# Kernel optimization log

Measured on AMD Instinct MI355X. Metric: run time of the kernel, lower is better.

## Reference

```python
import jax, jax.numpy as jnp
import numpy as np

B, N, D, K = 32, 4096, 128, 512
NPB = 2048          # unique tail nodes per batch (>= K so topk branch is taken)
M = B * NPB         # total unique tail nodes
E = B * N           # total edges
NUM_ENT = 10000


def setup_inputs() -> dict:
    key = jax.random.key(0)
    ks = jax.random.split(key, 18)
    f = lambda k, s: jax.random.normal(k, s, dtype=jnp.float32)
    inp = {
        "q_head": f(ks[0], (B, D)),
        "q_rel": f(ks[1], (B, D)),
        "q_time": f(ks[2], (B, D)),
        "r_neighbor": f(ks[3], (B, N, D)),
        "t_neighbor": f(ks[4], (B, N, D)),
        "time_neighbor": f(ks[5], (B, N, D)),
        "hidden": f(ks[6], (E, D)),
        "tail_emd": jnp.zeros((M, D), jnp.float32),  # scatter out-buffer
    }
    # tail_index: each edge of batch b scatters into that batch's node slab
    local = jax.random.randint(ks[7], (B, N), 0, NPB)
    inp["tail_index"] = (local + jnp.arange(B)[:, None] * NPB).reshape(E).astype(jnp.int32)
    # tail_nodes: [M,3] = (batch id, tail entity, time)
    batch_col = jnp.repeat(jnp.arange(B), NPB)
    tail_col = jax.random.randint(ks[8], (M,), 0, NUM_ENT)
    time_col = jax.random.randint(ks[9], (M,), 0, 365)
    inp["tail_nodes"] = jnp.stack([batch_col, tail_col, time_col], axis=-1).astype(jnp.int32)
    # linear-layer params (torch nn.Linear-style scaling)
    s3, s1 = 1.0 / np.sqrt(3 * D), 1.0 / np.sqrt(D)
    inp["W_q"] = f(ks[10], (3 * D, D)) * s3
    inp["b_q"] = jnp.zeros((D,), jnp.float32)
    inp["W_a"] = f(ks[11], (3 * D, D)) * s3
    inp["b_a"] = jnp.zeros((D,), jnp.float32)
    inp["W_att"] = f(ks[12], (3 * D, 1)) * s3
    inp["b_att"] = jnp.zeros((1,), jnp.float32)
    inp["W_rule"] = f(ks[13], (D, 1)) * s1
    inp["b_rule"] = jnp.zeros((1,), jnp.float32)
    inp["W_out"] = f(ks[14], (D, D)) * s1
    inp["b_out"] = jnp.zeros((D,), jnp.float32)
    return inp


def reference(q_head, q_rel, q_time, r_neighbor, t_neighbor, time_neighbor,
              hidden, tail_emd, tail_index, tail_nodes,
              W_q, b_q, W_a, b_a, W_att, b_att, W_rule, b_rule, W_out, b_out):
    # act = identity (module default). reduce = 'sum'.
    # raw message per edge: [E, D]
    message = (q_head[:, None, :] + r_neighbor + time_neighbor).reshape(E, D)
    # query / neighbor projections
    query = jnp.concatenate([q_head, q_rel, q_time], axis=-1) @ W_q + b_q      # [B, D]
    neigh = jnp.concatenate([r_neighbor, t_neighbor, time_neighbor], -1) @ W_a + b_a  # [B, N, D]
    q = query[:, None, :]
    qa = jnp.concatenate([q * neigh, q - neigh, q + neigh], axis=-1)           # [B, N, 3D]
    att1 = jax.nn.sigmoid(qa @ W_att + b_att).reshape(E, 1)
    att2 = jax.nn.sigmoid(hidden @ W_rule + b_rule)                            # [E, 1]
    att = (att1 + att2) * 0.5
    msg = att * message
    # scatter-sum aggregation over unique tail nodes
    seg = lambda v: jax.ops.segment_sum(v, tail_index, num_segments=M)
    tail_agg = tail_emd + seg(msg)            # scatter(..., out=tail_emd)
    new_hidden = seg(hidden)                  # [M, D]
    agg_att = seg(att[:, 0])                  # [M]
    # per-batch top-k over aggregated attention (each batch has NPB >= K nodes)
    nodes_batch = tail_nodes[:, 0]
    scores = jnp.where(nodes_batch[None, :] == jnp.arange(B)[:, None],
                       agg_att[None, :], -jnp.inf)                             # [B, M]
    _, idx = jax.lax.top_k(scores, K)                                          # [B, K] global node ids
    new_nodes = jnp.stack([tail_nodes[:, 1][idx], tail_nodes[:, 2][idx]], -1)  # [B, K, 2]
    emd = tail_agg[idx]                                                        # [B, K, D]
    hid = new_hidden[idx]                                                      # [B, K, D]
    out_emd = emd @ W_out + b_out                                              # act=identity
    return new_nodes, out_emd, hid
```

## Files before the change

### kernel.cpp

```cpp
#include <hip/hip_runtime.h>
#include <math.h>

#define B 32
#define N 4096
#define D 128
#define KTOP 512
#define NPB 2048
#define MSEG (B * NPB)
#define E (B * N)
#define MAXL 96

__global__ __launch_bounds__(128) void k0_precompute(
    const float* __restrict__ qh, const float* __restrict__ qr,
    const float* __restrict__ qt, const float* __restrict__ Wq,
    const float* __restrict__ bq, const float* __restrict__ Wa,
    const float* __restrict__ ba, const float* __restrict__ Watt,
    const float* __restrict__ batt, double* __restrict__ vws,
    double* __restrict__ c2ws) {
  int b = blockIdx.x, d = threadIdx.x;
  __shared__ double u[128];
  __shared__ double red[128];
  const float* qhb = qh + b * 128;
  const float* qrb = qr + b * 128;
  const float* qtb = qt + b * 128;
  double acc = (double)bq[d];
  for (int i = 0; i < 128; ++i) acc += (double)qhb[i] * (double)Wq[i * 128 + d];
  for (int i = 0; i < 128; ++i) acc += (double)qrb[i] * (double)Wq[(128 + i) * 128 + d];
  for (int i = 0; i < 128; ++i) acc += (double)qtb[i] * (double)Wq[(256 + i) * 128 + d];
  double w1 = (double)Watt[d], w2 = (double)Watt[128 + d], w3 = (double)Watt[256 + d];
  double ud = acc * w1 - w2 + w3;
  u[d] = ud;
  red[d] = acc * (w2 + w3) + (double)ba[d] * ud;
  __syncthreads();
  for (int s = 64; s > 0; s >>= 1) {
    if (d < s) red[d] += red[d + s];
    __syncthreads();
  }
  if (d == 0) c2ws[b] = red[0] + (double)batt[0];
  for (int i = d; i < 384; i += 128) {
    double vv = 0.0;
    for (int dd = 0; dd < 128; ++dd) vv += (double)Wa[i * 128 + dd] * u[dd];
    vws[b * 384 + i] = vv;
  }
}

__global__ __launch_bounds__(256) void k1_att(
    const float* __restrict__ r, const float* __restrict__ t,
    const float* __restrict__ tm, const float* __restrict__ hidden,
    const float* __restrict__ Wrule, const float* __restrict__ brule,
    const double* __restrict__ vws, const double* __restrict__ c2ws,
    float* __restrict__ attw) {
  int wid = threadIdx.x >> 6;
  int lane = threadIdx.x & 63;
  int e = blockIdx.x * 4 + wid;
  int b = e >> 12;
  size_t eo = (size_t)e * 128;
  const float2* r2 = (const float2*)(r + eo);
  const float2* t2 = (const float2*)(t + eo);
  const float2* m2 = (const float2*)(tm + eo);
  const float2* h2 = (const float2*)(hidden + eo);
  const double2* vb = (const double2*)(vws + b * 384);
  float2 ra = r2[lane], ta = t2[lane], ma = m2[lane], ha = h2[lane];
  double2 v0 = vb[lane], v1 = vb[64 + lane], v2 = vb[128 + lane];
  float2 wr = ((const float2*)Wrule)[lane];
  double p1 = (double)ra.x * v0.x + (double)ra.y * v0.y +
              (double)ta.x * v1.x + (double)ta.y * v1.y +
              (double)ma.x * v2.x + (double)ma.y * v2.y;
  double p2 = (double)ha.x * (double)wr.x + (double)ha.y * (double)wr.y;
  for (int off = 32; off > 0; off >>= 1) {
    p1 += __shfl_xor(p1, off);
    p2 += __shfl_xor(p2, off);
  }
  if (lane == 0) {
    double l1 = p1 + c2ws[b];
    double l2 = p2 + (double)brule[0];
    double a1 = 1.0 / (1.0 + exp(-l1));
    double a2 = 1.0 / (1.0 + exp(-l2));
    attw[e] = (float)(0.5 * (a1 + a2));
  }
}

__global__ __launch_bounds__(256) void k_hist(const int* __restrict__ tidx,
                                              int* __restrict__ counts) {
  int e = blockIdx.x * 256 + threadIdx.x;
  atomicAdd(&counts[tidx[e]], 1);
}

__global__ __launch_bounds__(256) void k_scanA(const int* __restrict__ counts,
                                               int* __restrict__ off,
                                               int* __restrict__ bsum) {
  __shared__ int sd[256];
  int tid = threadIdx.x;
  int g = blockIdx.x * 256 + tid;
  int c = counts[g];
  sd[tid] = c;
  __syncthreads();
  for (int s = 1; s < 256; s <<= 1) {
    int tv = (tid >= s) ? sd[tid - s] : 0;
    __syncthreads();
    sd[tid] += tv;
    __syncthreads();
  }
  off[g] = sd[tid] - c;
  if (tid == 255) bsum[blockIdx.x] = sd[255];
}

__global__ __launch_bounds__(256) void k_scanB(const int* __restrict__ bsum,
                                               int* __restrict__ boff) {
  __shared__ int sd[256];
  int tid = threadIdx.x;
  int c = bsum[tid];
  sd[tid] = c;
  __syncthreads();
  for (int s = 1; s < 256; s <<= 1) {
    int tv = (tid >= s) ? sd[tid - s] : 0;
    __syncthreads();
    sd[tid] += tv;
    __syncthreads();
  }
  boff[tid] = sd[tid] - c;
}

__global__ __launch_bounds__(256) void k_scanC(int* __restrict__ off,
                                               const int* __restrict__ boff,
                                               int* __restrict__ cur) {
  int g = blockIdx.x * 256 + threadIdx.x;
  int o = off[g] + boff[g >> 8];
  off[g] = o;
  cur[g] = o;
}

__global__ __launch_bounds__(256) void k_scatter(const int* __restrict__ tidx,
                                                 int* __restrict__ cur,
                                                 int* __restrict__ lists) {
  int e = blockIdx.x * 256 + threadIdx.x;
  int m = tidx[e];
  int pos = atomicAdd(&cur[m], 1);
  lists[pos] = e;
}

__global__ __launch_bounds__(128) void k5_agg(
    const float* __restrict__ r, const float* __restrict__ tm,
    const float* __restrict__ hidden, const float* __restrict__ qh,
    const float* __restrict__ tail_emd, const float* __restrict__ attw,
    const int* __restrict__ counts, const int* __restrict__ offs,
    const int* __restrict__ lists, float* __restrict__ tail_agg,
    float* __restrict__ new_hidden, float* __restrict__ agg_att) {
  int m = blockIdx.x;
  int d = threadIdx.x;
  int b = m >> 11;
  __shared__ int s_list[MAXL];
  __shared__ float s_att[MAXL];
  int cnt = counts[m];
  if (cnt > MAXL) cnt = MAXL;
  int off = offs[m];
  if (d < cnt) s_list[d] = lists[off + d];
  __syncthreads();
  if (d == 0) {
    for (int i = 1; i < cnt; i++) {
      int key = s_list[i];
      int j = i - 1;
      while (j >= 0 && s_list[j] > key) {
        s_list[j + 1] = s_list[j];
        j--;
      }
      s_list[j + 1] = key;
    }
  }
  __syncthreads();
  if (d < cnt) s_att[d] = attw[s_list[d]];
  __syncthreads();
  if (d == 0) {
    float s = 0.f;
    for (int j = 0; j < cnt; j++) s += s_att[j];
    agg_att[m] = s;
  }
  float qhd = qh[b * 128 + d];
  float accT = tail_emd[(size_t)m * 128 + d];
  float accH = 0.f;
  for (int j = 0; j < cnt; j++) {
    int e = s_list[j];
    float a = s_att[j];
    size_t eo = (size_t)e * 128 + d;
    float message = (qhd + r[eo]) + tm[eo];
    accT += a * message;
    accH += hidden[eo];
  }
  tail_agg[(size_t)m * 128 + d] = accT;
  new_hidden[(size_t)m * 128 + d] = accH;
}

__global__ __launch_bounds__(1024) void k6_topk(
    const float* __restrict__ agg_att, const int* __restrict__ tail_nodes,
    float* __restrict__ out_nodes, int* __restrict__ idxw) {
  __shared__ float v[2048];
  __shared__ int ix[2048];
  int b = blockIdx.x, tid = threadIdx.x;
  for (int s = tid; s < 2048; s += 1024) {
    v[s] = agg_att[b * 2048 + s];
    ix[s] = s;
  }
  __syncthreads();
  for (int k = 2; k <= 2048; k <<= 1) {
    for (int j = k >> 1; j > 0; j >>= 1) {
      for (int t = tid; t < 2048; t += 1024) {
        int p = t ^ j;
        if (p > t) {
          bool asc = ((t & k) == 0);
          float vt = v[t], vp = v[p];
          int it = ix[t], ip = ix[p];
          bool before_p = (vp > vt) || (vp == vt && ip < it);
          if (before_p == asc) {
            v[t] = vp; v[p] = vt;
            ix[t] = ip; ix[p] = it;
          }
        }
      }
      __syncthreads();
    }
  }
  if (tid < KTOP) {
    int s = ix[tid];
    int gm = b * 2048 + s;
    out_nodes[(b * KTOP + tid) * 2 + 0] = (float)tail_nodes[gm * 3 + 1];
    out_nodes[(b * KTOP + tid) * 2 + 1] = (float)tail_nodes[gm * 3 + 2];
    idxw[b * KTOP + tid] = gm;
  }
}

__global__ __launch_bounds__(256) void k7_out(
    const float* __restrict__ tail_agg, const float* __restrict__ new_hidden,
    const float* __restrict__ Wout, const float* __restrict__ bout,
    const int* __restrict__ idxw, float* __restrict__ out_emd,
    float* __restrict__ out_hid) {
  __shared__ float Ws[16384];
  __shared__ float es[256];
  int tid = threadIdx.x;
  int sub = tid >> 7, d = tid & 127;
  for (int i = tid; i < 16384; i += 256) Ws[i] = Wout[i];
  int base = blockIdx.x * 32;
  float bo = bout[d];
  for (int j = 0; j < 32; j += 2) {
    int row = base + j + sub;
    int m = idxw[row];
    __syncthreads();
    es[sub * 128 + d] = tail_agg[(size_t)m * 128 + d];
    __syncthreads();
    float acc = bo;
#pragma unroll 8
    for (int i = 0; i < 128; ++i) acc += es[sub * 128 + i] * Ws[i * 128 + d];
    out_emd[(size_t)row * 128 + d] = acc;
    out_hid[(size_t)row * 128 + d] = new_hidden[(size_t)m * 128 + d];
  }
}

extern "C" void kernel_launch(void* const* d_in, const int* in_sizes, int n_in,
                              void* d_out, int out_size, void* d_ws,
                              size_t ws_size, hipStream_t stream) {
  const float* q_head = (const float*)d_in[0];
  const float* q_rel = (const float*)d_in[1];
  const float* q_time = (const float*)d_in[2];
  const float* r_nb = (const float*)d_in[3];
  const float* t_nb = (const float*)d_in[4];
  const float* tm_nb = (const float*)d_in[5];
  const float* hidden = (const float*)d_in[6];
  const float* tail_emd = (const float*)d_in[7];
  const int* tail_index = (const int*)d_in[8];
  const int* tail_nodes = (const int*)d_in[9];
  const float* W_q = (const float*)d_in[10];
  const float* b_q = (const float*)d_in[11];
  const float* W_a = (const float*)d_in[12];
  const float* b_a = (const float*)d_in[13];
  const float* W_att = (const float*)d_in[14];
  const float* b_att = (const float*)d_in[15];
  const float* W_rule = (const float*)d_in[16];
  const float* b_rule = (const float*)d_in[17];
  const float* W_out = (const float*)d_in[18];
  const float* b_out = (const float*)d_in[19];

  char* ws = (char*)d_ws;
  double* vws = (double*)(ws + 0);
  double* c2ws = (double*)(ws + 98304);
  float* attw = (float*)(ws + 98560);
  int* counts = (int*)(ws + 622848);
  int* offs = (int*)(ws + 884992);
  int* cur = (int*)(ws + 1147136);
  int* bsum = (int*)(ws + 1409280);
  int* boff = (int*)(ws + 1410304);
  int* lists = (int*)(ws + 1411328);
  float* agg_att = (float*)(ws + 1935616);
  int* idxw = (int*)(ws + 2197760);
  float* tail_agg = (float*)(ws + 2263296);
  float* new_hid = (float*)(ws + 35817728);

  float* out_nodes = (float*)d_out;
  float* out_emd = (float*)d_out + (size_t)B * KTOP * 2;
  float* out_hid = out_emd + (size_t)B * KTOP * 128;

  k0_precompute<<<B, 128, 0, stream>>>(q_head, q_rel, q_time, W_q, b_q, W_a,
                                       b_a, W_att, b_att, vws, c2ws);
  k1_att<<<E / 4, 256, 0, stream>>>(r_nb, t_nb, tm_nb, hidden, W_rule, b_rule,
                                    vws, c2ws, attw);
  hipMemsetAsync(counts, 0, MSEG * sizeof(int), stream);
  k_hist<<<E / 256, 256, 0, stream>>>(tail_index, counts);
  k_scanA<<<MSEG / 256, 256, 0, stream>>>(counts, offs, bsum);
  k_scanB<<<1, 256, 0, stream>>>(bsum, boff);
  k_scanC<<<MSEG / 256, 256, 0, stream>>>(offs, boff, cur);
  k_scatter<<<E / 256, 256, 0, stream>>>(tail_index, cur, lists);
  k5_agg<<<MSEG, 128, 0, stream>>>(r_nb, tm_nb, hidden, q_head, tail_emd, attw,
                                   counts, offs, lists, tail_agg, new_hid,
                                   agg_att);
  k6_topk<<<B, 1024, 0, stream>>>(agg_att, tail_nodes, out_nodes, idxw);
  k7_out<<<(B * KTOP) / 32, 256, 0, stream>>>(tail_agg, new_hid, W_out, b_out,
                                              idxw, out_emd, out_hid);
}
```

Before: 495.3 us.

## Aggregate only top-k nodes, fixed-slot lists, rank-based topk, fp32 attention

Replaces the prefix-scan CSR build with fixed 32-slot per-node lists filled by atomics, and computes only the per-node attention sum before top-k. The full message and hidden aggregation now runs inside the output kernel, and only for the selected 512 nodes per batch, so the full-size tail_agg and new_hidden intermediates are never written. The attention kernel moves from double to float with float4 loads, and the bitonic sort is replaced by a parallel rank count spread over 8 blocks per batch. Risks: nodes with more than 32 edges are silently truncated, edge order in the sums is no longer deterministic, and float attention may change which nodes make the top-k.

```diff
diff --git a/kernel.cpp b/kernel.cpp
--- a/kernel.cpp
+++ b/kernel.cpp
@@ -8,7 +8,7 @@
 #define NPB 2048
 #define MSEG (B * NPB)
 #define E (B * N)
-#define MAXL 96
+#define MAXC 32
 
 __global__ __launch_bounds__(128) void k0_precompute(
     const float* __restrict__ qh, const float* __restrict__ qr,
@@ -16,7 +16,8 @@
     const float* __restrict__ bq, const float* __restrict__ Wa,
     const float* __restrict__ ba, const float* __restrict__ Watt,
     const float* __restrict__ batt, double* __restrict__ vws,
-    double* __restrict__ c2ws) {
+    double* __restrict__ c2ws, float* __restrict__ vf,
+    float* __restrict__ c2f) {
   int b = blockIdx.x, d = threadIdx.x;
   __shared__ double u[128];
   __shared__ double red[128];
@@ -36,11 +37,16 @@
     if (d < s) red[d] += red[d + s];
     __syncthreads();
   }
-  if (d == 0) c2ws[b] = red[0] + (double)batt[0];
+  if (d == 0) {
+    double c2 = red[0] + (double)batt[0];
+    c2ws[b] = c2;
+    c2f[b] = (float)c2;
+  }
   for (int i = d; i < 384; i += 128) {
     double vv = 0.0;
     for (int dd = 0; dd < 128; ++dd) vv += (double)Wa[i * 128 + dd] * u[dd];
     vws[b * 384 + i] = vv;
+    vf[b * 384 + i] = (float)vv;
   }
 }
 
@@ -48,188 +54,97 @@
     const float* __restrict__ r, const float* __restrict__ t,
     const float* __restrict__ tm, const float* __restrict__ hidden,
     const float* __restrict__ Wrule, const float* __restrict__ brule,
-    const double* __restrict__ vws, const double* __restrict__ c2ws,
+    const float* __restrict__ vf, const float* __restrict__ c2f,
     float* __restrict__ attw) {
-  int wid = threadIdx.x >> 6;
-  int lane = threadIdx.x & 63;
-  int e = blockIdx.x * 4 + wid;
-  int b = e >> 12;
-  size_t eo = (size_t)e * 128;
-  const float2* r2 = (const float2*)(r + eo);
-  const float2* t2 = (const float2*)(t + eo);
-  const float2* m2 = (const float2*)(tm + eo);
-  const float2* h2 = (const float2*)(hidden + eo);
-  const double2* vb = (const double2*)(vws + b * 384);
-  float2 ra = r2[lane], ta = t2[lane], ma = m2[lane], ha = h2[lane];
-  double2 v0 = vb[lane], v1 = vb[64 + lane], v2 = vb[128 + lane];
-  float2 wr = ((const float2*)Wrule)[lane];
-  double p1 = (double)ra.x * v0.x + (double)ra.y * v0.y +
-              (double)ta.x * v1.x + (double)ta.y * v1.y +
-              (double)ma.x * v2.x + (double)ma.y * v2.y;
-  double p2 = (double)ha.x * (double)wr.x + (double)ha.y * (double)wr.y;
-  for (int off = 32; off > 0; off >>= 1) {
-    p1 += __shfl_xor(p1, off);
-    p2 += __shfl_xor(p2, off);
-  }
-  if (lane == 0) {
-    double l1 = p1 + c2ws[b];
-    double l2 = p2 + (double)brule[0];
-    double a1 = 1.0 / (1.0 + exp(-l1));
-    double a2 = 1.0 / (1.0 + exp(-l2));
-    attw[e] = (float)(0.5 * (a1 + a2));
-  }
-}
-
-__global__ __launch_bounds__(256) void k_hist(const int* __restrict__ tidx,
-                                              int* __restrict__ counts) {
-  int e = blockIdx.x * 256 + threadIdx.x;
-  atomicAdd(&counts[tidx[e]], 1);
-}
-
-__global__ __launch_bounds__(256) void k_scanA(const int* __restrict__ counts,
-                                               int* __restrict__ off,
-                                               int* __restrict__ bsum) {
-  __shared__ int sd[256];
   int tid = threadIdx.x;
-  int g = blockIdx.x * 256 + tid;
-  int c = counts[g];
-  sd[tid] = c;
-  __syncthreads();
-  for (int s = 1; s < 256; s <<= 1) {
-    int tv = (tid >= s) ? sd[tid - s] : 0;
-    __syncthreads();
-    sd[tid] += tv;
-    __syncthreads();
-  }
-  off[g] = sd[tid] - c;
-  if (tid == 255) bsum[blockIdx.x] = sd[255];
-}
-
-__global__ __launch_bounds__(256) void k_scanB(const int* __restrict__ bsum,
-                                               int* __restrict__ boff) {
-  __shared__ int sd[256];
-  int tid = threadIdx.x;
-  int c = bsum[tid];
-  sd[tid] = c;
-  __syncthreads();
-  for (int s = 1; s < 256; s <<= 1) {
-    int tv = (tid >= s) ? sd[tid - s] : 0;
-    __syncthreads();
-    sd[tid] += tv;
-    __syncthreads();
-  }
-  boff[tid] = sd[tid] - c;
-}
-
-__global__ __launch_bounds__(256) void k_scanC(int* __restrict__ off,
-                                               const int* __restrict__ boff,
-                                               int* __restrict__ cur) {
-  int g = blockIdx.x * 256 + threadIdx.x;
-  int o = off[g] + boff[g >> 8];
-  off[g] = o;
-  cur[g] = o;
-}
-
-__global__ __launch_bounds__(256) void k_scatter(const int* __restrict__ tidx,
-                                                 int* __restrict__ cur,
-                                                 int* __restrict__ lists) {
+  int h = tid >> 5;
+  int l = tid & 31;
+  int base = blockIdx.x * 64;
+  int b = base >> 12;
+  const float4* vb = (const float4*)(vf + b * 384);
+  float4 v0 = vb[l];
+  float4 v1 = vb[32 + l];
+  float4 v2 = vb[64 + l];
+  float4 wr = ((const float4*)Wrule)[l];
+  float c2 = c2f[b];
+  float br = brule[0];
+#pragma unroll 4
+  for (int i = 0; i < 8; ++i) {
+    int e = base + i * 8 + h;
+    size_t eo = (size_t)e * 128 + l * 4;
+    float4 ra = *(const float4*)(r + eo);
+    float4 ta = *(const float4*)(t + eo);
+    float4 ma = *(const float4*)(tm + eo);
+    float4 ha = *(const float4*)(hidden + eo);
+    float p1 = ra.x * v0.x + ra.y * v0.y + ra.z * v0.z + ra.w * v0.w;
+    p1 += ta.x * v1.x + ta.y * v1.y + ta.z * v1.z + ta.w * v1.w;
+    p1 += ma.x * v2.x + ma.y * v2.y + ma.z * v2.z + ma.w * v2.w;
+    float p2 = ha.x * wr.x + ha.y * wr.y + ha.z * wr.z + ha.w * wr.w;
+#pragma unroll
+    for (int off = 16; off > 0; off >>= 1) {
+      p1 += __shfl_xor(p1, off);
+      p2 += __shfl_xor(p2, off);
+    }
+    if (l == 0) {
+      float a1 = 1.0f / (1.0f + expf(-(p1 + c2)));
+      float a2 = 1.0f / (1.0f + expf(-(p2 + br)));
+      attw[e] = 0.5f * (a1 + a2);
+    }
+  }
+}
+
+__global__ __launch_bounds__(256) void kb_build(const int* __restrict__ tidx,
+                                                int* __restrict__ counts,
+                                                int* __restrict__ lists) {
   int e = blockIdx.x * 256 + threadIdx.x;
   int m = tidx[e];
-  int pos = atomicAdd(&cur[m], 1);
-  lists[pos] = e;
-}
-
-__global__ __launch_bounds__(128) void k5_agg(
-    const float* __restrict__ r, const float* __restrict__ tm,
-    const float* __restrict__ hidden, const float* __restrict__ qh,
-    const float* __restrict__ tail_emd, const float* __restrict__ attw,
-    const int* __restrict__ counts, const int* __restrict__ offs,
-    const int* __restrict__ lists, float* __restrict__ tail_agg,
-    float* __restrict__ new_hidden, float* __restrict__ agg_att) {
-  int m = blockIdx.x;
-  int d = threadIdx.x;
-  int b = m >> 11;
-  __shared__ int s_list[MAXL];
-  __shared__ float s_att[MAXL];
+  int pos = atomicAdd(&counts[m], 1);
+  if (pos < MAXC) lists[m * MAXC + pos] = e;
+}
+
+__global__ __launch_bounds__(256) void k_agg(const int* __restrict__ counts,
+                                             const int* __restrict__ lists,
+                                             const float* __restrict__ attw,
+                                             float* __restrict__ agg_att) {
+  int m = blockIdx.x * 256 + threadIdx.x;
   int cnt = counts[m];
-  if (cnt > MAXL) cnt = MAXL;
-  int off = offs[m];
-  if (d < cnt) s_list[d] = lists[off + d];
-  __syncthreads();
-  if (d == 0) {
-    for (int i = 1; i < cnt; i++) {
-      int key = s_list[i];
-      int j = i - 1;
-      while (j >= 0 && s_list[j] > key) {
-        s_list[j + 1] = s_list[j];
-        j--;
-      }
-      s_list[j + 1] = key;
-    }
-  }
-  __syncthreads();
-  if (d < cnt) s_att[d] = attw[s_list[d]];
-  __syncthreads();
-  if (d == 0) {
-    float s = 0.f;
-    for (int j = 0; j < cnt; j++) s += s_att[j];
-    agg_att[m] = s;
-  }
-  float qhd = qh[b * 128 + d];
-  float accT = tail_emd[(size_t)m * 128 + d];
-  float accH = 0.f;
-  for (int j = 0; j < cnt; j++) {
-    int e = s_list[j];
-    float a = s_att[j];
-    size_t eo = (size_t)e * 128 + d;
-    float message = (qhd + r[eo]) + tm[eo];
-    accT += a * message;
-    accH += hidden[eo];
-  }
-  tail_agg[(size_t)m * 128 + d] = accT;
-  new_hidden[(size_t)m * 128 + d] = accH;
-}
-
-__global__ __launch_bounds__(1024) void k6_topk(
+  if (cnt > MAXC) cnt = MAXC;
+  float s = 0.f;
+  for (int j = 0; j < cnt; ++j) s += attw[lists[m * MAXC + j]];
+  agg_att[m] = s;
+}
+
+__global__ __launch_bounds__(256) void k6_topk(
     const float* __restrict__ agg_att, const int* __restrict__ tail_nodes,
     float* __restrict__ out_nodes, int* __restrict__ idxw) {
-  __shared__ float v[2048];
-  __shared__ int ix[2048];
-  int b = blockIdx.x, tid = threadIdx.x;
-  for (int s = tid; s < 2048; s += 1024) {
-    v[s] = agg_att[b * 2048 + s];
-    ix[s] = s;
-  }
+  __shared__ float sv[2048];
+  int b = blockIdx.x >> 3;
+  int chunk = blockIdx.x & 7;
+  int tid = threadIdx.x;
+  for (int s = tid; s < 2048; s += 256) sv[s] = agg_att[b * 2048 + s];
   __syncthreads();
-  for (int k = 2; k <= 2048; k <<= 1) {
-    for (int j = k >> 1; j > 0; j >>= 1) {
-      for (int t = tid; t < 2048; t += 1024) {
-        int p = t ^ j;
-        if (p > t) {
-          bool asc = ((t & k) == 0);
-          float vt = v[t], vp = v[p];
-          int it = ix[t], ip = ix[p];
-          bool before_p = (vp > vt) || (vp == vt && ip < it);
-          if (before_p == asc) {
-            v[t] = vp; v[p] = vt;
-            ix[t] = ip; ix[p] = it;
-          }
-        }
-      }
-      __syncthreads();
-    }
-  }
-  if (tid < KTOP) {
-    int s = ix[tid];
-    int gm = b * 2048 + s;
-    out_nodes[(b * KTOP + tid) * 2 + 0] = (float)tail_nodes[gm * 3 + 1];
-    out_nodes[(b * KTOP + tid) * 2 + 1] = (float)tail_nodes[gm * 3 + 2];
-    idxw[b * KTOP + tid] = gm;
+  int i = chunk * 256 + tid;
+  float vi = sv[i];
+  int rank = 0;
+#pragma unroll 8
+  for (int j = 0; j < 2048; ++j) {
+    float vj = sv[j];
+    rank += (vj > vi) || (vj == vi && j < i);
+  }
+  if (rank < KTOP) {
+    int gm = b * 2048 + i;
+    int p = b * KTOP + rank;
+    out_nodes[p * 2 + 0] = (float)tail_nodes[gm * 3 + 1];
+    out_nodes[p * 2 + 1] = (float)tail_nodes[gm * 3 + 2];
+    idxw[p] = gm;
   }
 }
 
 __global__ __launch_bounds__(256) void k7_out(
-    const float* __restrict__ tail_agg, const float* __restrict__ new_hidden,
+    const float* __restrict__ tail_emd, const float* __restrict__ r,
+    const float* __restrict__ tm, const float* __restrict__ hidden,
+    const float* __restrict__ qh, const float* __restrict__ attw,
+    const int* __restrict__ counts, const int* __restrict__ lists,
     const float* __restrict__ Wout, const float* __restrict__ bout,
     const int* __restrict__ idxw, float* __restrict__ out_emd,
     float* __restrict__ out_hid) {
@@ -243,14 +158,27 @@
   for (int j = 0; j < 32; j += 2) {
     int row = base + j + sub;
     int m = idxw[row];
+    int b = m >> 11;
+    int cnt = counts[m];
+    if (cnt > MAXC) cnt = MAXC;
+    float accT = tail_emd[(size_t)m * 128 + d];
+    float accH = 0.f;
+    float qhd = qh[b * 128 + d];
+    for (int jj = 0; jj < cnt; ++jj) {
+      int e = lists[m * MAXC + jj];
+      float a = attw[e];
+      size_t eo = (size_t)e * 128 + d;
+      accT += a * (qhd + r[eo] + tm[eo]);
+      accH += hidden[eo];
+    }
     __syncthreads();
-    es[sub * 128 + d] = tail_agg[(size_t)m * 128 + d];
+    es[sub * 128 + d] = accT;
     __syncthreads();
     float acc = bo;
 #pragma unroll 8
     for (int i = 0; i < 128; ++i) acc += es[sub * 128 + i] * Ws[i * 128 + d];
     out_emd[(size_t)row * 128 + d] = acc;
-    out_hid[(size_t)row * 128 + d] = new_hidden[(size_t)m * 128 + d];
+    out_hid[(size_t)row * 128 + d] = accH;
   }
 }
 
@@ -281,36 +209,28 @@
   char* ws = (char*)d_ws;
   double* vws = (double*)(ws + 0);
   double* c2ws = (double*)(ws + 98304);
-  float* attw = (float*)(ws + 98560);
-  int* counts = (int*)(ws + 622848);
-  int* offs = (int*)(ws + 884992);
-  int* cur = (int*)(ws + 1147136);
-  int* bsum = (int*)(ws + 1409280);
-  int* boff = (int*)(ws + 1410304);
-  int* lists = (int*)(ws + 1411328);
-  float* agg_att = (float*)(ws + 1935616);
-  int* idxw = (int*)(ws + 2197760);
-  float* tail_agg = (float*)(ws + 2263296);
-  float* new_hid = (float*)(ws + 35817728);
+  float* vf = (float*)(ws + 98560);
+  float* c2f = (float*)(ws + 147712);
+  float* attw = (float*)(ws + 147968);
+  int* counts = (int*)(ws + 672256);
+  int* lists = (int*)(ws + 934400);
+  float* agg_att = (float*)(ws + 9323008);
+  int* idxw = (int*)(ws + 9585152);
 
   float* out_nodes = (float*)d_out;
   float* out_emd = (float*)d_out + (size_t)B * KTOP * 2;
   float* out_hid = out_emd + (size_t)B * KTOP * 128;
 
+  hipMemsetAsync(counts, 0, MSEG * sizeof(int), stream);
   k0_precompute<<<B, 128, 0, stream>>>(q_head, q_rel, q_time, W_q, b_q, W_a,
-                                       b_a, W_att, b_att, vws, c2ws);
-  k1_att<<<E / 4, 256, 0, stream>>>(r_nb, t_nb, tm_nb, hidden, W_rule, b_rule,
-                                    vws, c2ws, attw);
-  hipMemsetAsync(counts, 0, MSEG * sizeof(int), stream);
-  k_hist<<<E / 256, 256, 0, stream>>>(tail_index, counts);
-  k_scanA<<<MSEG / 256, 256, 0, stream>>>(counts, offs, bsum);
-  k_scanB<<<1, 256, 0, stream>>>(bsum, boff);
-  k_scanC<<<MSEG / 256, 256, 0, stream>>>(offs, boff, cur);
-  k_scatter<<<E / 256, 256, 0, stream>>>(tail_index, cur, lists);
-  k5_agg<<<MSEG, 128, 0, stream>>>(r_nb, tm_nb, hidden, q_head, tail_emd, attw,
-                                   counts, offs, lists, tail_agg, new_hid,
-                                   agg_att);
-  k6_topk<<<B, 1024, 0, stream>>>(agg_att, tail_nodes, out_nodes, idxw);
-  k7_out<<<(B * KTOP) / 32, 256, 0, stream>>>(tail_agg, new_hid, W_out, b_out,
-                                              idxw, out_emd, out_hid);
-}
+                                       b_a, W_att, b_att, vws, c2ws, vf, c2f);
+  k1_att<<<E / 64, 256, 0, stream>>>(r_nb, t_nb, tm_nb, hidden, W_rule, b_rule,
+                                     vf, c2f, attw);
+  kb_build<<<E / 256, 256, 0, stream>>>(tail_index, counts, lists);
+  k_agg<<<MSEG / 256, 256, 0, stream>>>(counts, lists, attw, agg_att);
+  k6_topk<<<B * 8, 256, 0, stream>>>(agg_att, tail_nodes, out_nodes, idxw);
+  k7_out<<<(B * KTOP) / 32, 256, 0, stream>>>(tail_emd, r_nb, tm_nb, hidden,
+                                              q_head, attw, counts, lists,
+                                              W_out, b_out, idxw, out_emd,
+                                              out_hid);
+}
```

New measurement: 501.3 us. Within noise of the previous version (+1.2%).
